# Kernel tuning notes

Measured on AMD Instinct MI355X. Metric: run time of the kernel, lower is better.

## Reference

```python
import jax, jax.numpy as jnp
import numpy as np

N_HEADS = 16
EMBED = 1024
SEQ = 2048
BATCH = 4
GELU_C = 0.044715
EPS = 1e-5


def gelu_tanh(x):
    return 0.5 * x * (1.0 + jnp.tanh(jnp.sqrt(2.0 / jnp.pi) * (x + GELU_C * x ** 3)))


def layer_norm(x, scale, shift):
    mean = jnp.mean(x, axis=-1, keepdims=True)
    var = jnp.var(x, axis=-1, keepdims=True)
    return scale * (x - mean) / jnp.sqrt(var + EPS) + shift


def setup_inputs() -> dict:
    key = jax.random.key(0)
    ks = jax.random.split(key, 8)
    d = EMBED
    s = 0.02
    return {
        "X": jax.random.normal(ks[0], (BATCH, SEQ, d), dtype=jnp.float32),
        "Wq": jax.random.normal(ks[1], (d, d), dtype=jnp.float32) * s,
        "Wk": jax.random.normal(ks[2], (d, d), dtype=jnp.float32) * s,
        "Wv": jax.random.normal(ks[3], (d, d), dtype=jnp.float32) * s,
        "Wo": jax.random.normal(ks[4], (d, d), dtype=jnp.float32) * s,
        "W1": jax.random.normal(ks[5], (d, 4 * d), dtype=jnp.float32) * s,
        "b1": jnp.zeros((4 * d,), dtype=jnp.float32),
        "W2": jax.random.normal(ks[6], (4 * d, d), dtype=jnp.float32) * s,
        "b2": jnp.zeros((d,), dtype=jnp.float32),
        "ln1_scale": jnp.ones((d,), dtype=jnp.float32),
        "ln1_shift": jnp.zeros((d,), dtype=jnp.float32),
        "ln2_scale": jnp.ones((d,), dtype=jnp.float32),
        "ln2_shift": jnp.zeros((d,), dtype=jnp.float32),
    }


def attention(x, Wq, Wk, Wv, Wo):
    b, s, d = x.shape
    h, dh = N_HEADS, d // N_HEADS
    q = (x @ Wq).reshape(b, s, h, dh).transpose(0, 2, 1, 3)  # [b,h,s,dh]
    k = (x @ Wk).reshape(b, s, h, dh).transpose(0, 2, 1, 3)
    v = (x @ Wv).reshape(b, s, h, dh).transpose(0, 2, 1, 3)
    scores = jnp.einsum("bhqd,bhkd->bhqk", q, k) / jnp.sqrt(jnp.float32(dh))
    causal = jnp.tril(jnp.ones((s, s), dtype=bool))
    scores = jnp.where(causal, scores, -jnp.inf)
    w = jax.nn.softmax(scores, axis=-1)  # dropout rate 0 -> identity
    ctx = jnp.einsum("bhqk,bhkd->bhqd", w, v)
    ctx = ctx.transpose(0, 2, 1, 3).reshape(b, s, d)
    return ctx @ Wo


def reference(X, Wq, Wk, Wv, Wo, W1, b1, W2, b2,
              ln1_scale, ln1_shift, ln2_scale, ln2_shift):
    h = layer_norm(X, ln1_scale, ln1_shift)
    X = X + attention(h, Wq, Wk, Wv, Wo)
    h = layer_norm(X, ln2_scale, ln2_shift)
    h = gelu_tanh(h @ W1 + b1) @ W2 + b2
    return X + h
```

## Files before the change

### kernel.cpp

```cpp
#include <hip/hip_runtime.h>

typedef unsigned short u16;
typedef __attribute__((ext_vector_type(8))) short bf16x8;
typedef __attribute__((ext_vector_type(4))) float fx4;

#define MFMA16(a, b, c) __builtin_amdgcn_mfma_f32_16x16x32_bf16((a), (b), (c), 0, 0, 0)

__device__ __forceinline__ u16 f2bf(float f) {
  unsigned u = __float_as_uint(f);
  u += 0x7fffu + ((u >> 16) & 1u);
  return (u16)(u >> 16);
}

__device__ __forceinline__ void gload_lds16(const void* g, void* l) {
  __builtin_amdgcn_global_load_lds((const __attribute__((address_space(1))) void*)g,
                                   (__attribute__((address_space(3))) void*)l,
                                   16, 0, 0);
}

struct WP {
  const float* s[6];
  u16* d[6];
};
__global__ __launch_bounds__(256) void tcvt_all(WP p) {
  __shared__ float t[32][33];
  const int id = blockIdx.x;
  int which, bx, by, R, C;
  if (id < 4096) {
    which = id >> 10;
    const int q = id & 1023;
    bx = q >> 5; by = q & 31; R = 1024; C = 1024;
  } else if (id < 8192) {
    which = 4;
    const int q = id - 4096;
    bx = q & 127; by = q >> 7; R = 1024; C = 4096;
  } else {
    which = 5;
    const int q = id - 8192;
    bx = q & 31; by = q >> 5; R = 4096; C = 1024;
  }
  const float* src = p.s[which];
  u16* dst = p.d[which];
  const int tx = threadIdx.x & 31, ty = threadIdx.x >> 5;
#pragma unroll
  for (int i = 0; i < 4; ++i)
    t[ty + i * 8][tx] = src[(size_t)(by * 32 + ty + i * 8) * C + bx * 32 + tx];
  __syncthreads();
#pragma unroll
  for (int i = 0; i < 4; ++i)
    dst[(size_t)(bx * 32 + ty + i * 8) * R + by * 32 + tx] = f2bf(t[tx][ty + i * 8]);
}

__global__ __launch_bounds__(256) void ln_kernel(const float* __restrict__ x,
                                                 const float* __restrict__ sc,
                                                 const float* __restrict__ sh,
                                                 u16* __restrict__ out) {
  const int row = blockIdx.x, tid = threadIdx.x;
  const float4 v = ((const float4*)(x + (size_t)row * 1024))[tid];
  float s = v.x + v.y + v.z + v.w;
  float ss = v.x * v.x + v.y * v.y + v.z * v.z + v.w * v.w;
#pragma unroll
  for (int d = 32; d >= 1; d >>= 1) {
    s += __shfl_xor(s, d);
    ss += __shfl_xor(ss, d);
  }
  __shared__ float rs[4], rq[4];
  const int w = tid >> 6;
  if ((tid & 63) == 0) { rs[w] = s; rq[w] = ss; }
  __syncthreads();
  s = rs[0] + rs[1] + rs[2] + rs[3];
  ss = rq[0] + rq[1] + rq[2] + rq[3];
  const float mean = s * (1.f / 1024.f);
  const float var = ss * (1.f / 1024.f) - mean * mean;
  const float rstd = rsqrtf(var + 1e-5f);
  const float4 g = ((const float4*)sc)[tid];
  const float4 b = ((const float4*)sh)[tid];
  ushort4 o;
  o.x = f2bf(g.x * (v.x - mean) * rstd + b.x);
  o.y = f2bf(g.y * (v.y - mean) * rstd + b.y);
  o.z = f2bf(g.z * (v.z - mean) * rstd + b.z);
  o.w = f2bf(g.w * (v.w - mean) * rstd + b.w);
  ((ushort4*)(out + (size_t)row * 1024))[tid] = o;
}

template <int MODE>
__global__ __launch_bounds__(512, 1) void gemm256(
    const u16* __restrict__ A, const u16* __restrict__ Bt, int K,
    void* __restrict__ outp, const float* __restrict__ aux,
    u16* __restrict__ qd, u16* __restrict__ kd, u16* __restrict__ vd) {
  __shared__ u16 lds[2][2][256 * 64];
  const int tid = threadIdx.x;
  const int lane = tid & 63, w = tid >> 6;
  const int lo = lane & 15, hi = lane >> 4;
  const int wm = w >> 2, wn = w & 3;
  const int tM = blockIdx.y * 256, tN = blockIdx.x * 256;
  const int NT = K >> 6;

  const int rb = tid >> 3;
  const int uc = ((tid & 7) ^ (rb & 7)) * 8;

#define STGH(BUFI, XI, XPTR, TOFF, H, KK)                                        \
  do {                                                                           \
    _Pragma("unroll") for (int ph = 0; ph < 2; ++ph) {                           \
      const int rl = (H) * 128 + ph * 64 + rb;                                   \
      gload_lds16(XPTR + (size_t)((TOFF) + rl) * K + (KK) + uc,                  \
                  &lds[BUFI][XI][(H) * 8192 + ph * 4096 + tid * 8]);             \
    }                                                                            \
  } while (0)

  fx4 acc[8][4];
#pragma unroll
  for (int m = 0; m < 8; ++m)
#pragma unroll
    for (int n = 0; n < 4; ++n) acc[m][n] = (fx4){0.f, 0.f, 0.f, 0.f};

#pragma unroll
  for (int pt = 0; pt < 2; ++pt) {
    STGH(pt, 0, A, tM, 0, pt * 64);
    STGH(pt, 0, A, tM, 1, pt * 64);
    STGH(pt, 1, Bt, tN, 0, pt * 64);
    STGH(pt, 1, Bt, tN, 1, pt * 64);
  }

  for (int t = 0; t < NT; ++t) {
    const int bi = t & 1;
    const u16* bufA = &lds[bi][0][0];
    const u16* bufB = &lds[bi][1][0];
    if (t == NT - 1) {
      asm volatile("s_waitcnt vmcnt(0)" ::: "memory");
    } else {
      asm volatile("s_waitcnt vmcnt(8)" ::: "memory");
    }
    __builtin_amdgcn_s_barrier();

    bf16x8 bfr[4][2], afr[4][2];
#pragma unroll
    for (int n = 0; n < 4; ++n)
#pragma unroll
      for (int ks = 0; ks < 2; ++ks) {
        const int R = wn * 64 + n * 16 + lo;
        bfr[n][ks] = *(const bf16x8*)&bufB[R * 64 + (((ks << 2) + hi) ^ (R & 7)) * 8];
      }
#pragma unroll
    for (int m = 0; m < 4; ++m)
#pragma unroll
      for (int ks = 0; ks < 2; ++ks) {
        const int R = wm * 128 + m * 16 + lo;
        afr[m][ks] = *(const bf16x8*)&bufA[R * 64 + (((ks << 2) + hi) ^ (R & 7)) * 8];
      }
    asm volatile("s_waitcnt lgkmcnt(0)" ::: "memory");
    __builtin_amdgcn_sched_barrier(0);
    __builtin_amdgcn_s_barrier();
    if (t + 2 < NT) {
      STGH(bi, 1, Bt, tN, 0, (t + 2) * 64);
      STGH(bi, 1, Bt, tN, 1, (t + 2) * 64);
    }
    bf16x8 afr2[4][2];
#pragma unroll
    for (int m = 0; m < 4; ++m)
#pragma unroll
      for (int ks = 0; ks < 2; ++ks) {
        const int R = wm * 128 + (m + 4) * 16 + lo;
        afr2[m][ks] = *(const bf16x8*)&bufA[R * 64 + (((ks << 2) + hi) ^ (R & 7)) * 8];
      }
    __builtin_amdgcn_s_setprio(1);
#pragma unroll
    for (int m = 0; m < 4; ++m)
#pragma unroll
      for (int n = 0; n < 4; ++n) {
        acc[m][n] = MFMA16(afr[m][0], bfr[n][0], acc[m][n]);
        acc[m][n] = MFMA16(afr[m][1], bfr[n][1], acc[m][n]);
      }
    __builtin_amdgcn_s_setprio(0);
    asm volatile("s_waitcnt lgkmcnt(0)" ::: "memory");
    __builtin_amdgcn_sched_barrier(0);
    __builtin_amdgcn_s_barrier();
    if (t + 2 < NT) {
      STGH(bi, 0, A, tM, 0, (t + 2) * 64);
      STGH(bi, 0, A, tM, 1, (t + 2) * 64);
    }
    __builtin_amdgcn_s_setprio(1);
#pragma unroll
    for (int m = 0; m < 4; ++m)
#pragma unroll
      for (int n = 0; n < 4; ++n) {
        acc[m + 4][n] = MFMA16(afr2[m][0], bfr[n][0], acc[m + 4][n]);
        acc[m + 4][n] = MFMA16(afr2[m][1], bfr[n][1], acc[m + 4][n]);
      }
    __builtin_amdgcn_s_setprio(0);
  }
#undef STGH

#pragma unroll
  for (int m = 0; m < 8; ++m) {
    const int rgb = tM + wm * 128 + m * 16 + hi * 4;
#pragma unroll
    for (int n = 0; n < 4; ++n) {
      const int cg = tN + wn * 64 + n * 16 + lo;
#pragma unroll
      for (int r = 0; r < 4; ++r) {
        const float v = acc[m][n][r];
        const int rg = rgb + r;
        if constexpr (MODE == 0) {
          const int which = cg >> 10, c = cg & 1023;
          const int head = c >> 6, dhi = c & 63;
          const int b = rg >> 11, sidx = rg & 2047;
          const int bh = b * 16 + head;
          const u16 bv = f2bf(v);
          if (which == 0)      qd[((size_t)bh * 2048 + sidx) * 64 + dhi] = bv;
          else if (which == 1) kd[((size_t)bh * 2048 + sidx) * 64 + dhi] = bv;
          else                 vd[((size_t)bh * 64 + dhi) * 2048 + sidx] = bv;
        } else {
          const float xx = v + aux[cg];
          const float t2 = xx + 0.044715f * xx * xx * xx;
          const float e = __expf(1.5957691216057308f * t2);
          const float th = 1.f - 2.f / (e + 1.f);
          ((u16*)outp)[(size_t)rg * 4096 + cg] = f2bf(0.5f * xx * (1.f + th));
        }
      }
    }
  }
}

template <int MODE>
__global__ __launch_bounds__(512, 1) void gemm256x128(
    const u16* __restrict__ A, const u16* __restrict__ Bt, int K,
    float* __restrict__ outp, const float* __restrict__ aux) {
  __shared__ u16 lA[2][256 * 64];
  __shared__ u16 lB[2][128 * 64];
  const int tid = threadIdx.x;
  const int lane = tid & 63, w = tid >> 6;
  const int lo = lane & 15, hi = lane >> 4;
  const int wm = w >> 1, wn = w & 1;
  const int tM = blockIdx.y * 256, tN = blockIdx.x * 128;
  const int NT = K >> 6;

  const int rb = tid >> 3;
  const int uc = ((tid & 7) ^ (rb & 7)) * 8;

#define STGA(BUFI, KK)                                                  \
  do {                                                                  \
    _Pragma("unroll") for (int i = 0; i < 4; ++i) {                     \
      gload_lds16(A + (size_t)(tM + i * 64 + rb) * K + (KK) + uc,       \
                  &lA[BUFI][i * 4096 + tid * 8]);                       \
    }                                                                   \
  } while (0)
#define STGB(BUFI, KK)                                                  \
  do {                                                                  \
    _Pragma("unroll") for (int i = 0; i < 2; ++i) {                     \
      gload_lds16(Bt + (size_t)(tN + i * 64 + rb) * K + (KK) + uc,      \
                  &lB[BUFI][i * 4096 + tid * 8]);                       \
    }                                                                   \
  } while (0)

  fx4 acc[4][4];
#pragma unroll
  for (int m = 0; m < 4; ++m)
#pragma unroll
    for (int n = 0; n < 4; ++n) acc[m][n] = (fx4){0.f, 0.f, 0.f, 0.f};

  STGA(0, 0);
  STGB(0, 0);
  STGA(1, 64);
  STGB(1, 64);

  for (int t = 0; t < NT; ++t) {
    const int bi = t & 1;
    const u16* bufA = &lA[bi][0];
    const u16* bufB = &lB[bi][0];
    if (t == NT - 1) {
      asm volatile("s_waitcnt vmcnt(0)" ::: "memory");
    } else {
      asm volatile("s_waitcnt vmcnt(6)" ::: "memory");
    }
    __builtin_amdgcn_s_barrier();

    bf16x8 bfr[4][2], af1[2][2];
#pragma unroll
    for (int n = 0; n < 4; ++n)
#pragma unroll
      for (int ks = 0; ks < 2; ++ks) {
        const int R = wn * 64 + n * 16 + lo;
        bfr[n][ks] = *(const bf16x8*)&bufB[R * 64 + (((ks << 2) + hi) ^ (R & 7)) * 8];
      }
#pragma unroll
    for (int m = 0; m < 2; ++m)
#pragma unroll
      for (int ks = 0; ks < 2; ++ks) {
        const int R = wm * 64 + m * 16 + lo;
        af1[m][ks] = *(const bf16x8*)&bufA[R * 64 + (((ks << 2) + hi) ^ (R & 7)) * 8];
      }
    asm volatile("s_waitcnt lgkmcnt(0)" ::: "memory");
    __builtin_amdgcn_sched_barrier(0);
    __builtin_amdgcn_s_barrier();
    if (t + 2 < NT) STGB(bi, (t + 2) * 64);
    bf16x8 af2[2][2];
#pragma unroll
    for (int m = 0; m < 2; ++m)
#pragma unroll
      for (int ks = 0; ks < 2; ++ks) {
        const int R = wm * 64 + (m + 2) * 16 + lo;
        af2[m][ks] = *(const bf16x8*)&bufA[R * 64 + (((ks << 2) + hi) ^ (R & 7)) * 8];
      }
    __builtin_amdgcn_s_setprio(1);
#pragma unroll
    for (int m = 0; m < 2; ++m)
#pragma unroll
      for (int n = 0; n < 4; ++n) {
        acc[m][n] = MFMA16(af1[m][0], bfr[n][0], acc[m][n]);
        acc[m][n] = MFMA16(af1[m][1], bfr[n][1], acc[m][n]);
      }
    __builtin_amdgcn_s_setprio(0);
    asm volatile("s_waitcnt lgkmcnt(0)" ::: "memory");
    __builtin_amdgcn_sched_barrier(0);
    __builtin_amdgcn_s_barrier();
    if (t + 2 < NT) STGA(bi, (t + 2) * 64);
    __builtin_amdgcn_s_setprio(1);
#pragma unroll
    for (int m = 0; m < 2; ++m)
#pragma unroll
      for (int n = 0; n < 4; ++n) {
        acc[m + 2][n] = MFMA16(af2[m][0], bfr[n][0], acc[m + 2][n]);
        acc[m + 2][n] = MFMA16(af2[m][1], bfr[n][1], acc[m + 2][n]);
      }
    __builtin_amdgcn_s_setprio(0);
  }
#undef STGA
#undef STGB

#pragma unroll
  for (int m = 0; m < 4; ++m) {
    const int rgb = tM + wm * 64 + m * 16 + hi * 4;
#pragma unroll
    for (int n = 0; n < 4; ++n) {
      const int cg = tN + wn * 64 + n * 16 + lo;
#pragma unroll
      for (int r = 0; r < 4; ++r) {
        const float v = acc[m][n][r];
        const int rg = rgb + r;
        const size_t idx = (size_t)rg * 1024 + cg;
        if constexpr (MODE == 1) {
          outp[idx] = aux[idx] + v;
        } else {
          outp[idx] = outp[idx] + v + aux[cg];
        }
      }
    }
  }
}

__global__ __launch_bounds__(512) void attn_kernel(const u16* __restrict__ Q,
                                                   const u16* __restrict__ Kg,
                                                   const u16* __restrict__ Vt,
                                                   u16* __restrict__ ctx) {
  __shared__ u16 lK[2][64 * 64];
  __shared__ u16 lV[2][64 * 64];
  __shared__ u16 Plds[8][16 * 64];
  const int tid = threadIdx.x;
  const int w = tid >> 6, lane = tid & 63;
  const int lo = lane & 15, hi = lane >> 4;
  const int bh = blockIdx.x;
  const int j = blockIdx.y;
  const u16* Qb = Q + (size_t)bh * 2048 * 64;
  const u16* Kb = Kg + (size_t)bh * 2048 * 64;
  const u16* Vb = Vt + (size_t)bh * 64 * 2048;
  u16* Pw = Plds[w];
  const int nt0 = 2 * j + 2;

  const int rowS = tid >> 3;
  const int ugS = (tid & 7) ^ (rowS & 7);

#define STAGE(BUF, KB)                                                         \
  do {                                                                         \
    gload_lds16(Kb + (size_t)((KB) + rowS) * 64 + ugS * 8, &lK[BUF][tid * 8]); \
    gload_lds16(Vb + (size_t)rowS * 2048 + (KB) + ugS * 8, &lV[BUF][tid * 8]); \
  } while (0)

  const int b = bh >> 4, h = bh & 15;
  const float SCALE = 0.18033688011112042f;

  int qt = j;
  int qw = qt * 128 + w * 16;

  bf16x8 qf[2];
#pragma unroll
  for (int kc = 0; kc < 2; ++kc)
    qf[kc] = *(const bf16x8*)&Qb[(size_t)(qw + lo) * 64 + kc * 32 + hi * 8];

  fx4 accO[4];
  float mrow[4], lrow[4];
#pragma unroll
  for (int t2 = 0; t2 < 4; ++t2) {
    accO[t2] = (fx4){0.f, 0.f, 0.f, 0.f};
    mrow[t2] = -1e30f;
    lrow[t2] = 0.f;
  }

  STAGE(0, 0);
  __syncthreads();

  int buf = 0;
  for (int t = 0; t < 34; ++t) {
    if (t + 1 < 34) {
      const int tn = t + 1;
      const int kbn = (tn < nt0 ? tn : tn - nt0) * 64;
      STAGE(buf ^ 1, kbn);
    }
    if (t == nt0) {
#pragma unroll
      for (int t2 = 0; t2 < 4; ++t2)
#pragma unroll
        for (int r = 0; r < 4; ++r) {
          const int rg = b * 2048 + qw + hi * 4 + r;
          const int cg = h * 64 + t2 * 16 + lo;
          ctx[(size_t)rg * 1024 + cg] = f2bf(accO[t2][r] / lrow[r]);
        }
      qt = 15 - j;
      qw = qt * 128 + w * 16;
#pragma unroll
      for (int kc = 0; kc < 2; ++kc)
        qf[kc] = *(const bf16x8*)&Qb[(size_t)(qw + lo) * 64 + kc * 32 + hi * 8];
#pragma unroll
      for (int t2 = 0; t2 < 4; ++t2) {
        accO[t2] = (fx4){0.f, 0.f, 0.f, 0.f};
        mrow[t2] = -1e30f;
        lrow[t2] = 0.f;
      }
    }
    const int kb = (t < nt0 ? t : t - nt0) * 64;
    if (kb <= qw + 15) {
      const u16* lKb = lK[buf];
      const u16* lVb = lV[buf];
      fx4 s[4];
#pragma unroll
      for (int tt = 0; tt < 4; ++tt) {
        const int r = tt * 16 + lo;
        const bf16x8 kf0 = *(const bf16x8*)&lKb[r * 64 + ((hi ^ (r & 7)) << 3)];
        const bf16x8 kf1 = *(const bf16x8*)&lKb[r * 64 + (((4 + hi) ^ (r & 7)) << 3)];
        fx4 z = (fx4){0.f, 0.f, 0.f, 0.f};
        z = MFMA16(qf[0], kf0, z);
        z = MFMA16(qf[1], kf1, z);
        s[tt] = z;
      }
      if (kb + 63 > qw) {
#pragma unroll
        for (int tt = 0; tt < 4; ++tt)
#pragma unroll
          for (int r = 0; r < 4; ++r) {
            const int key = kb + tt * 16 + lo;
            const int qr = qw + hi * 4 + r;
            s[tt][r] = (key > qr) ? -1e30f : s[tt][r] * SCALE;
          }
      } else {
#pragma unroll
        for (int tt = 0; tt < 4; ++tt)
#pragma unroll
          for (int r = 0; r < 4; ++r) s[tt][r] *= SCALE;
      }
      float mt[4];
#pragma unroll
      for (int r = 0; r < 4; ++r)
        mt[r] = fmaxf(fmaxf(s[0][r], s[1][r]), fmaxf(s[2][r], s[3][r]));
#pragma unroll
      for (int d = 8; d >= 1; d >>= 1)
#pragma unroll
        for (int r = 0; r < 4; ++r) mt[r] = fmaxf(mt[r], __shfl_xor(mt[r], d));
      bool ok = true;
#pragma unroll
      for (int r = 0; r < 4; ++r) ok = ok && (mt[r] <= mrow[r] + 8.f);
      if (!__all(ok)) {
#pragma unroll
        for (int r = 0; r < 4; ++r) {
          const float mn = fmaxf(mrow[r], mt[r]);
          const float fsc = exp2f(mrow[r] - mn);
          mrow[r] = mn;
          lrow[r] *= fsc;
#pragma unroll
          for (int t2 = 0; t2 < 4; ++t2) accO[t2][r] *= fsc;
        }
      }
      float la[4] = {0.f, 0.f, 0.f, 0.f};
#pragma unroll
      for (int tt = 0; tt < 4; ++tt)
#pragma unroll
        for (int r = 0; r < 4; ++r) {
          const float p = exp2f(s[tt][r] - mrow[r]);
          s[tt][r] = p;
          la[r] += p;
        }
#pragma unroll
      for (int d = 8; d >= 1; d >>= 1)
#pragma unroll
        for (int r = 0; r < 4; ++r) la[r] += __shfl_xor(la[r], d);
#pragma unroll
      for (int r = 0; r < 4; ++r) lrow[r] += la[r];
#pragma unroll
      for (int tt = 0; tt < 4; ++tt)
#pragma unroll
        for (int r = 0; r < 4; ++r) {
          const int row = hi * 4 + r;
          const int colB = (tt * 16 + lo) * 2;
          Pw[(row * 128 + (colB ^ ((row & 7) << 4))) >> 1] = f2bf(s[tt][r]);
        }
      asm volatile("s_waitcnt lgkmcnt(0)" ::: "memory");
      bf16x8 pf[2];
#pragma unroll
      for (int kc = 0; kc < 2; ++kc) {
        const int row = lo;
        const int colB = kc * 64 + hi * 16;
        pf[kc] = *(const bf16x8*)((const char*)Pw + row * 128 + (colB ^ ((row & 7) << 4)));
      }
#pragma unroll
      for (int t2 = 0; t2 < 4; ++t2) {
        const int r2 = t2 * 16 + lo;
        const bf16x8 vf0 = *(const bf16x8*)&lVb[r2 * 64 + ((hi ^ (r2 & 7)) << 3)];
        const bf16x8 vf1 = *(const bf16x8*)&lVb[r2 * 64 + (((4 + hi) ^ (r2 & 7)) << 3)];
        accO[t2] = MFMA16(pf[0], vf0, accO[t2]);
        accO[t2] = MFMA16(pf[1], vf1, accO[t2]);
      }
    }
    __syncthreads();
    buf ^= 1;
  }
#pragma unroll
  for (int t2 = 0; t2 < 4; ++t2)
#pragma unroll
    for (int r = 0; r < 4; ++r) {
      const int rg = b * 2048 + qw + hi * 4 + r;
      const int cg = h * 64 + t2 * 16 + lo;
      ctx[(size_t)rg * 1024 + cg] = f2bf(accO[t2][r] / lrow[r]);
    }
#undef STAGE
}

extern "C" void kernel_launch(void* const* d_in, const int* in_sizes, int n_in,
                              void* d_out, int out_size, void* d_ws, size_t ws_size,
                              hipStream_t stream) {
  const float* X    = (const float*)d_in[0];
  const float* Wq   = (const float*)d_in[1];
  const float* Wk   = (const float*)d_in[2];
  const float* Wv   = (const float*)d_in[3];
  const float* Wo   = (const float*)d_in[4];
  const float* W1   = (const float*)d_in[5];
  const float* b1   = (const float*)d_in[6];
  const float* W2   = (const float*)d_in[7];
  const float* b2   = (const float*)d_in[8];
  const float* ln1s = (const float*)d_in[9];
  const float* ln1b = (const float*)d_in[10];
  const float* ln2s = (const float*)d_in[11];
  const float* ln2b = (const float*)d_in[12];

  const size_t SZ_WQKVT = 3072UL * 1024;
  const size_t SZ_WOT   = 1024UL * 1024;
  const size_t SZ_W1T   = 4096UL * 1024;
  const size_t SZ_W2T   = 1024UL * 4096;
  const size_t SZ_H     = 8192UL * 1024;
  const size_t SZ_QKV   = 64UL * 2048 * 64;

  u16* WqkvT = (u16*)d_ws;
  u16* WoT   = WqkvT + SZ_WQKVT;
  u16* W1T   = WoT + SZ_WOT;
  u16* W2T   = W1T + SZ_W1T;
  u16* hbuf  = W2T + SZ_W2T;
  u16* qbuf  = hbuf + SZ_H;
  u16* kbuf  = qbuf + SZ_QKV;
  u16* vbuf  = kbuf + SZ_QKV;
  u16* gbuf  = vbuf + SZ_QKV;
  u16* ctx   = hbuf;
  u16* h2    = qbuf;

  float* out = (float*)d_out;
  dim3 blk(256);

  WP wp;
  wp.s[0] = Wq; wp.s[1] = Wk; wp.s[2] = Wv; wp.s[3] = Wo; wp.s[4] = W1; wp.s[5] = W2;
  wp.d[0] = WqkvT;
  wp.d[1] = WqkvT + 1024 * 1024;
  wp.d[2] = WqkvT + 2 * 1024 * 1024;
  wp.d[3] = WoT;
  wp.d[4] = W1T;
  wp.d[5] = W2T;
  tcvt_all<<<12288, blk, 0, stream>>>(wp);

  ln_kernel<<<8192, blk, 0, stream>>>(X, ln1s, ln1b, hbuf);
  gemm256<0><<<dim3(12, 32), dim3(512), 0, stream>>>(hbuf, WqkvT, 1024,
                                                     nullptr, nullptr, qbuf, kbuf, vbuf);
  attn_kernel<<<dim3(64, 8), dim3(512), 0, stream>>>(qbuf, kbuf, vbuf, ctx);
  gemm256x128<1><<<dim3(8, 32), dim3(512), 0, stream>>>(ctx, WoT, 1024, out, X);
  ln_kernel<<<8192, blk, 0, stream>>>(out, ln2s, ln2b, h2);
  gemm256<2><<<dim3(16, 32), dim3(512), 0, stream>>>(h2, W1T, 1024,
                                                     gbuf, b1, nullptr, nullptr, nullptr);
  gemm256x128<3><<<dim3(8, 32), dim3(512), 0, stream>>>(gbuf, W2T, 4096, out, b2);
}
```

Baseline: 489.6 us.

## Reorder GEMM main loops to overlap MFMA with LDS reads; retile QKV projection

Both GEMM kernels now issue the first half of the MFMAs right after the fragment loads, with no lgkmcnt(0) wait in between, so LDS reads overlap with tensor-core math. The second MFMA half now runs before the barrier that precedes the next A-tile prefetch. The QKV projection moves from the 256x256 kernel to the 256x128 kernel with a 24x32 grid, which gives more blocks across the CUs. The intent is to reduce stalls on LDS reads and to improve occupancy and load balance for the QKV GEMM. The tradeoff is a smaller output tile per block for QKV, which lowers data reuse.

```diff
diff --git a/kernel.cpp b/kernel.cpp
--- a/kernel.cpp
+++ b/kernel.cpp
@@ -132,6 +132,7 @@
       asm volatile("s_waitcnt vmcnt(8)" ::: "memory");
     }
     __builtin_amdgcn_s_barrier();
+    __builtin_amdgcn_sched_barrier(0);
 
     bf16x8 bfr[4][2], afr[4][2];
 #pragma unroll
@@ -148,9 +149,18 @@
         const int R = wm * 128 + m * 16 + lo;
         afr[m][ks] = *(const bf16x8*)&bufA[R * 64 + (((ks << 2) + hi) ^ (R & 7)) * 8];
       }
-    asm volatile("s_waitcnt lgkmcnt(0)" ::: "memory");
+    __builtin_amdgcn_s_setprio(1);
+#pragma unroll
+    for (int m = 0; m < 4; ++m)
+#pragma unroll
+      for (int n = 0; n < 4; ++n) {
+        acc[m][n] = MFMA16(afr[m][0], bfr[n][0], acc[m][n]);
+        acc[m][n] = MFMA16(afr[m][1], bfr[n][1], acc[m][n]);
+      }
+    __builtin_amdgcn_s_setprio(0);
     __builtin_amdgcn_sched_barrier(0);
     __builtin_amdgcn_s_barrier();
+    __builtin_amdgcn_sched_barrier(0);
     if (t + 2 < NT) {
       STGH(bi, 1, Bt, tN, 0, (t + 2) * 64);
       STGH(bi, 1, Bt, tN, 1, (t + 2) * 64);
@@ -168,26 +178,17 @@
     for (int m = 0; m < 4; ++m)
 #pragma unroll
       for (int n = 0; n < 4; ++n) {
-        acc[m][n] = MFMA16(afr[m][0], bfr[n][0], acc[m][n]);
-        acc[m][n] = MFMA16(afr[m][1], bfr[n][1], acc[m][n]);
+        acc[m + 4][n] = MFMA16(afr2[m][0], bfr[n][0], acc[m + 4][n]);
+        acc[m + 4][n] = MFMA16(afr2[m][1], bfr[n][1], acc[m + 4][n]);
       }
     __builtin_amdgcn_s_setprio(0);
-    asm volatile("s_waitcnt lgkmcnt(0)" ::: "memory");
     __builtin_amdgcn_sched_barrier(0);
     __builtin_amdgcn_s_barrier();
+    __builtin_amdgcn_sched_barrier(0);
     if (t + 2 < NT) {
       STGH(bi, 0, A, tM, 0, (t + 2) * 64);
       STGH(bi, 0, A, tM, 1, (t + 2) * 64);
     }
-    __builtin_amdgcn_s_setprio(1);
-#pragma unroll
-    for (int m = 0; m < 4; ++m)
-#pragma unroll
-      for (int n = 0; n < 4; ++n) {
-        acc[m + 4][n] = MFMA16(afr2[m][0], bfr[n][0], acc[m + 4][n]);
-        acc[m + 4][n] = MFMA16(afr2[m][1], bfr[n][1], acc[m + 4][n]);
-      }
-    __builtin_amdgcn_s_setprio(0);
   }
 #undef STGH
 
@@ -201,22 +202,11 @@
       for (int r = 0; r < 4; ++r) {
         const float v = acc[m][n][r];
         const int rg = rgb + r;
-        if constexpr (MODE == 0) {
-          const int which = cg >> 10, c = cg & 1023;
-          const int head = c >> 6, dhi = c & 63;
-          const int b = rg >> 11, sidx = rg & 2047;
-          const int bh = b * 16 + head;
-          const u16 bv = f2bf(v);
-          if (which == 0)      qd[((size_t)bh * 2048 + sidx) * 64 + dhi] = bv;
-          else if (which == 1) kd[((size_t)bh * 2048 + sidx) * 64 + dhi] = bv;
-          else                 vd[((size_t)bh * 64 + dhi) * 2048 + sidx] = bv;
-        } else {
-          const float xx = v + aux[cg];
-          const float t2 = xx + 0.044715f * xx * xx * xx;
-          const float e = __expf(1.5957691216057308f * t2);
-          const float th = 1.f - 2.f / (e + 1.f);
-          ((u16*)outp)[(size_t)rg * 4096 + cg] = f2bf(0.5f * xx * (1.f + th));
-        }
+        const float xx = v + aux[cg];
+        const float t2 = xx + 0.044715f * xx * xx * xx;
+        const float e = __expf(1.5957691216057308f * t2);
+        const float th = 1.f - 2.f / (e + 1.f);
+        ((u16*)outp)[(size_t)rg * 4096 + cg] = f2bf(0.5f * xx * (1.f + th));
       }
     }
   }
@@ -225,7 +215,8 @@
 template <int MODE>
 __global__ __launch_bounds__(512, 1) void gemm256x128(
     const u16* __restrict__ A, const u16* __restrict__ Bt, int K,
-    float* __restrict__ outp, const float* __restrict__ aux) {
+    void* __restrict__ outp, const float* __restrict__ aux,
+    u16* __restrict__ qd, u16* __restrict__ kd, u16* __restrict__ vd) {
   __shared__ u16 lA[2][256 * 64];
   __shared__ u16 lB[2][128 * 64];
   const int tid = threadIdx.x;
@@ -274,6 +265,7 @@
       asm volatile("s_waitcnt vmcnt(6)" ::: "memory");
     }
     __builtin_amdgcn_s_barrier();
+    __builtin_amdgcn_sched_barrier(0);
 
     bf16x8 bfr[4][2], af1[2][2];
 #pragma unroll
@@ -290,9 +282,18 @@
         const int R = wm * 64 + m * 16 + lo;
         af1[m][ks] = *(const bf16x8*)&bufA[R * 64 + (((ks << 2) + hi) ^ (R & 7)) * 8];
       }
-    asm volatile("s_waitcnt lgkmcnt(0)" ::: "memory");
+    __builtin_amdgcn_s_setprio(1);
+#pragma unroll
+    for (int m = 0; m < 2; ++m)
+#pragma unroll
+      for (int n = 0; n < 4; ++n) {
+        acc[m][n] = MFMA16(af1[m][0], bfr[n][0], acc[m][n]);
+        acc[m][n] = MFMA16(af1[m][1], bfr[n][1], acc[m][n]);
+      }
+    __builtin_amdgcn_s_setprio(0);
     __builtin_amdgcn_sched_barrier(0);
     __builtin_amdgcn_s_barrier();
+    __builtin_amdgcn_sched_barrier(0);
     if (t + 2 < NT) STGB(bi, (t + 2) * 64);
     bf16x8 af2[2][2];
 #pragma unroll
@@ -307,23 +308,14 @@
     for (int m = 0; m < 2; ++m)
 #pragma unroll
       for (int n = 0; n < 4; ++n) {
-        acc[m][n] = MFMA16(af1[m][0], bfr[n][0], acc[m][n]);
-        acc[m][n] = MFMA16(af1[m][1], bfr[n][1], acc[m][n]);
-      }
-    __builtin_amdgcn_s_setprio(0);
-    asm volatile("s_waitcnt lgkmcnt(0)" ::: "memory");
-    __builtin_amdgcn_sched_barrier(0);
-    __builtin_amdgcn_s_barrier();
-    if (t + 2 < NT) STGA(bi, (t + 2) * 64);
-    __builtin_amdgcn_s_setprio(1);
-#pragma unroll
-    for (int m = 0; m < 2; ++m)
-#pragma unroll
-      for (int n = 0; n < 4; ++n) {
         acc[m + 2][n] = MFMA16(af2[m][0], bfr[n][0], acc[m + 2][n]);
         acc[m + 2][n] = MFMA16(af2[m][1], bfr[n][1], acc[m + 2][n]);
       }
     __builtin_amdgcn_s_setprio(0);
+    __builtin_amdgcn_sched_barrier(0);
+    __builtin_amdgcn_s_barrier();
+    __builtin_amdgcn_sched_barrier(0);
+    if (t + 2 < NT) STGA(bi, (t + 2) * 64);
   }
 #undef STGA
 #undef STGB
@@ -338,11 +330,23 @@
       for (int r = 0; r < 4; ++r) {
         const float v = acc[m][n][r];
         const int rg = rgb + r;
-        const size_t idx = (size_t)rg * 1024 + cg;
-        if constexpr (MODE == 1) {
-          outp[idx] = aux[idx] + v;
+        if constexpr (MODE == 0) {
+          const int which = cg >> 10, c = cg & 1023;
+          const int head = c >> 6, dhi = c & 63;
+          const int b = rg >> 11, sidx = rg & 2047;
+          const int bh = b * 16 + head;
+          const u16 bv = f2bf(v);
+          if (which == 0)      qd[((size_t)bh * 2048 + sidx) * 64 + dhi] = bv;
+          else if (which == 1) kd[((size_t)bh * 2048 + sidx) * 64 + dhi] = bv;
+          else                 vd[((size_t)bh * 64 + dhi) * 2048 + sidx] = bv;
+        } else if constexpr (MODE == 1) {
+          float* o = (float*)outp;
+          const size_t idx = (size_t)rg * 1024 + cg;
+          o[idx] = aux[idx] + v;
         } else {
-          outp[idx] = outp[idx] + v + aux[cg];
+          float* o = (float*)outp;
+          const size_t idx = (size_t)rg * 1024 + cg;
+          o[idx] = o[idx] + v + aux[cg];
         }
       }
     }
@@ -583,12 +587,14 @@
   tcvt_all<<<12288, blk, 0, stream>>>(wp);
 
   ln_kernel<<<8192, blk, 0, stream>>>(X, ln1s, ln1b, hbuf);
-  gemm256<0><<<dim3(12, 32), dim3(512), 0, stream>>>(hbuf, WqkvT, 1024,
-                                                     nullptr, nullptr, qbuf, kbuf, vbuf);
+  gemm256x128<0><<<dim3(24, 32), dim3(512), 0, stream>>>(hbuf, WqkvT, 1024,
+                                                         nullptr, nullptr, qbuf, kbuf, vbuf);
   attn_kernel<<<dim3(64, 8), dim3(512), 0, stream>>>(qbuf, kbuf, vbuf, ctx);
-  gemm256x128<1><<<dim3(8, 32), dim3(512), 0, stream>>>(ctx, WoT, 1024, out, X);
+  gemm256x128<1><<<dim3(8, 32), dim3(512), 0, stream>>>(ctx, WoT, 1024,
+                                                        out, X, nullptr, nullptr, nullptr);
   ln_kernel<<<8192, blk, 0, stream>>>(out, ln2s, ln2b, h2);
   gemm256<2><<<dim3(16, 32), dim3(512), 0, stream>>>(h2, W1T, 1024,
                                                      gbuf, b1, nullptr, nullptr, nullptr);
-  gemm256x128<3><<<dim3(8, 32), dim3(512), 0, stream>>>(gbuf, W2T, 4096, out, b2);
-}
+  gemm256x128<3><<<dim3(8, 32), dim3(512), 0, stream>>>(gbuf, W2T, 4096,
+                                                        out, b2, nullptr, nullptr, nullptr);
+}
```

Result: slower. 515.3 us (+5.3%).
